# Performance work log

Hardware: AMD Instinct MI355X
Metric: run time of the kernel (lower is better)

Reference implementation:

```python
import jax, jax.numpy as jnp
import numpy as np

B, N, K = 32, 2048, 32768  # batch, flattened neurons, number of unstable (I.sum()) rows


def setup_inputs() -> dict:
    key = jax.random.key(0)
    k1, k2, k3, k4, k5 = jax.random.split(key, 5)
    batch_idx = jnp.sort(jax.random.randint(k1, (K,), 0, B)).astype(jnp.int32)   # I_ind[:,0]
    neuron_idx = jax.random.randint(k2, (K,), 0, N).astype(jnp.int32)            # I_ind[:,1]
    d_vals = jax.random.normal(k3, (K,), dtype=jnp.float32)                      # d[I]
    d_next = jax.random.normal(k4, (B, N), dtype=jnp.float32)                    # next layer's d
    zlI = jax.random.normal(k5, (K,), dtype=jnp.float32)                         # zl[I]
    return {"batch_idx": batch_idx, "neuron_idx": neuron_idx,
            "d_vals": d_vals, "d_next": d_next, "zlI": zlI}


def reference(batch_idx, neuron_idx, d_vals, d_next, zlI):
    k = d_vals.shape[0]
    b, n = d_next.shape
    # __init__: scatter-build sparse indicator nus: nu[r, neuron_idx[r]] = d_vals[r]
    nu = jnp.zeros((k, n), dtype=d_vals.dtype).at[jnp.arange(k), neuron_idx].set(d_vals)
    # apply -> DualReLU.affine(..., I_ind): gather d rows by batch index, elementwise multiply
    nu = d_next[batch_idx] * nu  # [K, n]
    # fval (nu_prev=None): clamp then segment-sum over batch index.
    # Original emulates the segment reduction with a dense [K,B] one-hot I_collapse matmul;
    # segment_sum is the exact, efficient equivalent.
    zl = jax.ops.segment_sum(zlI[:, None] * jnp.maximum(-nu, 0.0), batch_idx,
                             num_segments=b, indices_are_sorted=True)   # [B, n]
    zu = -jax.ops.segment_sum(zlI[:, None] * jnp.maximum(nu, 0.0), batch_idx,
                              num_segments=b, indices_are_sorted=True)  # [B, n]
    return jnp.stack([zl, zu])  # [2, B, n]
```

## Files before the change

kernel.cpp:

```cpp
#include <hip/hip_runtime.h>


__global__ __launch_bounds__(1024) void dualrelu_scatter_kernel(
    const int*   __restrict__ batch_idx,
    const int*   __restrict__ neuron_idx,
    const float* __restrict__ d_vals,
    const float* __restrict__ d_next,
    const float* __restrict__ zlI,
    float*       __restrict__ out,
    int K, int B, int N)
{
    extern __shared__ float lds[];
    float* zl = lds;
    float* zu = lds + N;

    const int b    = blockIdx.x;
    const int tid  = threadIdx.x;
    const int nthr = blockDim.x;

    for (int i = tid; i < 2 * N; i += nthr) lds[i] = 0.0f;

    int lo, hi;
    {
        int l = 0, r = K;
        while (l < r) { int m = (l + r) >> 1; if (batch_idx[m] < b)     l = m + 1; else r = m; }
        lo = l;
        r = K;
        while (l < r) { int m = (l + r) >> 1; if (batch_idx[m] < b + 1) l = m + 1; else r = m; }
        hi = l;
    }
    __syncthreads();

    const float* __restrict__ drow = d_next + (size_t)b * N;

    for (int r = lo + tid; r < hi; r += nthr) {
        int   n = neuron_idx[r];
        float v = drow[n] * d_vals[r];
        float add = -zlI[r] * v;
        if (v < 0.0f)      atomicAdd(&zl[n], add);
        else if (v > 0.0f) atomicAdd(&zu[n], add);
    }
    __syncthreads();

    float* __restrict__ outzl = out + (size_t)b * N;
    float* __restrict__ outzu = out + (size_t)(B + b) * N;
    for (int i = tid; i < N; i += nthr) {
        outzl[i] = zl[i];
        outzu[i] = zu[i];
    }
}

extern "C" void kernel_launch(void* const* d_in, const int* in_sizes, int n_in,
                              void* d_out, int out_size, void* d_ws, size_t ws_size,
                              hipStream_t stream) {
    const int*   batch_idx  = (const int*)  d_in[0];
    const int*   neuron_idx = (const int*)  d_in[1];
    const float* d_vals     = (const float*)d_in[2];
    const float* d_next     = (const float*)d_in[3];
    const float* zlI        = (const float*)d_in[4];
    float*       out        = (float*)d_out;

    const int K = in_sizes[0];
    const int B = 32;
    const int N = in_sizes[3] / B;

    dim3 grid(B), block(1024);
    size_t lds_bytes = (size_t)2 * N * sizeof(float);
    dualrelu_scatter_kernel<<<grid, block, lds_bytes, stream>>>(
        batch_idx, neuron_idx, d_vals, d_next, zlI, out, K, B, N);
}
```

Before: 10.97 us.

## Replace serial per-thread binary search with cooperative two-level segment search

Each thread previously ran two serial binary searches over batch_idx, a chain of dependent global loads. Now the block samples batch_idx at strided probes, finds the coarse bucket in LDS, then two wavefronts scan that bucket in parallel to find the exact segment bounds. The d_next row is also staged into LDS for the gather, and the output write is vectorised to float4. The change adds extra barriers and assumes N is divisible by 4.

Result: faster. 9.609 us (-12.4%).

```diff
diff --git a/kernel.cpp b/kernel.cpp
--- a/kernel.cpp
+++ b/kernel.cpp
@@ -1,52 +1,92 @@
 #include <hip/hip_runtime.h>
+#include <limits.h>
 
 
-__global__ __launch_bounds__(1024) void dualrelu_scatter_kernel(
+#define NTHR 1024
+
+__global__ __launch_bounds__(NTHR) void dualrelu_kernel(
     const int*   __restrict__ batch_idx,
     const int*   __restrict__ neuron_idx,
     const float* __restrict__ d_vals,
     const float* __restrict__ d_next,
     const float* __restrict__ zlI,
     float*       __restrict__ out,
-    int K, int B, int N)
+    int K, int B, int N, int S)
 {
-    extern __shared__ float lds[];
-    float* zl = lds;
-    float* zu = lds + N;
+    extern __shared__ char smem[];
+    float* drow   = (float*)smem;
+    float* zl     = drow + N;
+    float* zu     = zl + N;
+    int*   probes = (int*)(zu + N);
+    int*   ctrl   = probes + NTHR;
 
-    const int b    = blockIdx.x;
-    const int tid  = threadIdx.x;
-    const int nthr = blockDim.x;
+    const int b   = blockIdx.x;
+    const int tid = threadIdx.x;
 
-    for (int i = tid; i < 2 * N; i += nthr) lds[i] = 0.0f;
+    int ppos  = tid * S;
+    int probe = (ppos < K) ? batch_idx[ppos] : INT_MAX;
 
-    int lo, hi;
+    const int N2 = N >> 1;
+    const float2* __restrict__ dg2 = (const float2*)(d_next + (size_t)b * N);
+    float2* drow2 = (float2*)drow;
+
+    if (tid == 0) { ctrl[0] = -1; ctrl[1] = -1; ctrl[2] = 0; ctrl[3] = 0; }
+    for (int i = tid; i < 2 * N; i += NTHR) zl[i] = 0.0f;
+
+    for (int i = tid; i < N2; i += NTHR) drow2[i] = dg2[i];
+    probes[tid] = probe;
+    __syncthreads();
+
     {
-        int l = 0, r = K;
-        while (l < r) { int m = (l + r) >> 1; if (batch_idx[m] < b)     l = m + 1; else r = m; }
-        lo = l;
-        r = K;
-        while (l < r) { int m = (l + r) >> 1; if (batch_idx[m] < b + 1) l = m + 1; else r = m; }
-        hi = l;
+        int a = probes[tid];
+        int c = (tid < NTHR - 1) ? probes[tid + 1] : INT_MAX;
+        if (a < b     && c >= b    ) ctrl[0] = tid;
+        if (a < b + 1 && c >= b + 1) ctrl[1] = tid;
     }
     __syncthreads();
 
-    const float* __restrict__ drow = d_next + (size_t)b * N;
+    {
+        int wave = tid >> 6;
+        int lane = tid & 63;
+        if (wave < 2) {
+            int thr_v = b + wave;
+            int w = ctrl[wave];
+            if (w >= 0) {
+                for (int j = lane; j < S; j += 64) {
+                    int p  = w * S + 1 + j;
+                    int v  = (p     < K) ? batch_idx[p]     : INT_MAX;
+                    int pv = (p - 1 < K) ? batch_idx[p - 1] : INT_MAX;
+                    if (pv < thr_v && v >= thr_v) ctrl[2 + wave] = p;
+                }
+            }
+        }
+    }
+    __syncthreads();
 
-    for (int r = lo + tid; r < hi; r += nthr) {
-        int   n = neuron_idx[r];
-        float v = drow[n] * d_vals[r];
-        float add = -zlI[r] * v;
+    const int lo = ctrl[2];
+    const int hi = ctrl[3];
+
+    for (int r = lo + tid; r < hi; r += NTHR) {
+        int   n  = neuron_idx[r];
+        float dv = d_vals[r];
+        float z  = zlI[r];
+        float v  = drow[n] * dv;
+        float add = -z * v;
         if (v < 0.0f)      atomicAdd(&zl[n], add);
         else if (v > 0.0f) atomicAdd(&zu[n], add);
     }
     __syncthreads();
 
-    float* __restrict__ outzl = out + (size_t)b * N;
-    float* __restrict__ outzu = out + (size_t)(B + b) * N;
-    for (int i = tid; i < N; i += nthr) {
-        outzl[i] = zl[i];
-        outzu[i] = zu[i];
+    const int N4 = N >> 2;
+    const float4* zl4 = (const float4*)zl;
+    const float4* zu4 = (const float4*)zu;
+    float4* ozl = (float4*)(out + (size_t)b * N);
+    float4* ozu = (float4*)(out + (size_t)(B + b) * N);
+    if (N4 == (NTHR >> 1)) {
+        if (tid < N4) ozl[tid]       = zl4[tid];
+        else          ozu[tid - N4]  = zu4[tid - N4];
+    } else {
+        for (int i = tid; i < N4; i += NTHR) { ozl[i] = zl4[i]; ozu[i] = zu4[i]; }
     }
 }
 
@@ -63,9 +103,9 @@
     const int K = in_sizes[0];
     const int B = 32;
     const int N = in_sizes[3] / B;
+    const int S = (K + NTHR - 1) / NTHR;
 
-    dim3 grid(B), block(1024);
-    size_t lds_bytes = (size_t)2 * N * sizeof(float);
-    dualrelu_scatter_kernel<<<grid, block, lds_bytes, stream>>>(
-        batch_idx, neuron_idx, d_vals, d_next, zlI, out, K, B, N);
+    size_t lds_bytes = (size_t)3 * N * sizeof(float) + (NTHR + 4) * sizeof(int);
+    dualrelu_kernel<<<dim3(B), dim3(NTHR), lds_bytes, stream>>>(
+        batch_idx, neuron_idx, d_vals, d_next, zlI, out, K, B, N, S);
 }
```
